# Optimization experiments

Hardware: AMD Instinct MI355X
Metric: run time of the kernel (lower is better)

The kernel has to match this reference:

```python
import jax, jax.numpy as jnp
import numpy as np

B, S, H = 32, 4096, 512

def setup_inputs() -> dict:
    key = jax.random.key(0)
    k1, k2, k3, k4, k5 = jax.random.split(key, 5)
    scale = 1.0 / np.sqrt(H)
    return {
        "query": jax.random.normal(k1, (B, 1, H), dtype=jnp.float32),
        "keys": jax.random.normal(k2, (B, S, H), dtype=jnp.float32),
        "Wa": jax.random.normal(k3, (H, H), dtype=jnp.float32) * scale,
        "Ua": jax.random.normal(k4, (H, H), dtype=jnp.float32) * scale,
        "Va": jax.random.normal(k5, (H, 1), dtype=jnp.float32) * scale,
    }

def reference(query, keys, Wa, Ua, Va):
    # additive (Bahdanau) attention scores: Va^T tanh(Wa q + Ua k)
    q_proj = jnp.einsum('bqh,hd->bqd', query, Wa)          # [B,1,H]
    k_proj = jnp.einsum('bsh,hd->bsd', keys, Ua)           # [B,S,H]
    scores = jnp.einsum('bsd,d->bs', jnp.tanh(q_proj + k_proj), Va[:, 0])  # [B,S]
    weights = jax.nn.softmax(scores, axis=-1)[:, None, :]  # [B,1,S]
    context = jnp.einsum('bqs,bsh->bqh', weights, keys)    # [B,1,H]
    return (context, weights)
```

## Files before the change

### kernel.cpp

```cpp
#include <hip/hip_runtime.h>
#include <hip/hip_bf16.h>

#define B_ 32
#define S_ 4096
#define H_ 512

typedef short bf16x8 __attribute__((ext_vector_type(8)));
typedef unsigned short u16x8 __attribute__((ext_vector_type(8)));
typedef float f32x4 __attribute__((ext_vector_type(4)));

__device__ inline unsigned short f2bf(float x) {
    unsigned u = __float_as_uint(x);
    return (unsigned short)((u + 0x7fffu + ((u >> 16) & 1u)) >> 16);
}

__device__ inline float fast_tanh(float x) {
    float e = __expf(2.f * x);
    return 1.f - 2.f / (e + 1.f);
}

__device__ __forceinline__ void stage16(const void* g, void* lds_base) {
    __builtin_amdgcn_global_load_lds(
        (const __attribute__((address_space(1))) unsigned char*)g,
        (__attribute__((address_space(3))) unsigned char*)lds_base, 16, 0, 0);
}

__global__ void k_prep_ua(const float* __restrict__ Ua,
                          unsigned short* __restrict__ ua_t) {
    __shared__ float tile[32][33];
    int h0 = blockIdx.x * 32, d0 = blockIdx.y * 32;
    int tx = threadIdx.x, ty = threadIdx.y;
#pragma unroll
    for (int j = 0; j < 4; ++j)
        tile[ty + j * 8][tx] = Ua[(size_t)(h0 + ty + j * 8) * H_ + d0 + tx];
    __syncthreads();
#pragma unroll
    for (int j = 0; j < 4; ++j) {
        int dl = ty + j * 8;
        ua_t[(size_t)(d0 + dl) * H_ + h0 + tx] = f2bf(tile[tx][dl]);
    }
}

__global__ __launch_bounds__(512) void k_qproj(const float* __restrict__ query,
                                               const float* __restrict__ Wa,
                                               float* __restrict__ qproj) {
    __shared__ float q[H_];
    int b = blockIdx.x, d = threadIdx.x;
    q[d] = query[(size_t)b * H_ + d];
    __syncthreads();
    float acc = 0.f;
    for (int h = 0; h < H_; ++h)
        acc = fmaf(q[h], Wa[(size_t)h * H_ + d], acc);
    qproj[(size_t)b * H_ + d] = acc;
}

__global__ __launch_bounds__(512, 2) void k_scores(
    const float* __restrict__ keys, const unsigned short* __restrict__ ua_t,
    const float* __restrict__ qproj, const float* __restrict__ Va,
    float* __restrict__ part_sc) {
    __shared__ __align__(16) unsigned char As[2][16384];
    __shared__ __align__(16) unsigned char Bs[2][16384];
    __shared__ float smp[4][128];

    int tid = threadIdx.x;
    int wave = tid >> 6, lane = tid & 63;
    int lq = lane & 15, lh = lane >> 4;
    int wm = wave >> 2;
    int wnn = wave & 3;

    int logical = (blockIdx.x & 7) * 512 + (blockIdx.x >> 3);
    int b  = logical >> 7;
    int m0 = ((logical >> 2) & 31) * 128;
    int nb = logical & 3;

    const float* keysb = keys + (size_t)b * S_ * H_;

    int r = tid >> 2, qtr = tid & 3;
    const float* aptr = keysb + (size_t)(m0 + r) * H_ + qtr * 16;
    unsigned aswz  = (unsigned)((r & 7) << 4);
    unsigned abase = (unsigned)(r * 128);

    int rb0 = wave * 8 + (lane >> 3);
    int rb1 = 64 + rb0;
    unsigned cb = (unsigned)((lane & 7) * 16);
    const unsigned char* uab = (const unsigned char*)ua_t;
    const unsigned char* bsrc0 = uab + ((size_t)(nb * 128 + rb0)) * 1024 + (cb ^ ((rb0 & 7) << 4));
    const unsigned char* bsrc1 = uab + ((size_t)(nb * 128 + rb1)) * 1024 + (cb ^ ((rb1 & 7) << 4));

    f32x4 acc[4][2];
#pragma unroll
    for (int i = 0; i < 4; ++i)
#pragma unroll
        for (int j = 0; j < 2; ++j) acc[i][j] = (f32x4){0.f, 0.f, 0.f, 0.f};

    unsigned swzR = (unsigned)((lq & 7) << 4);

    float4 arg[4];

    stage16(bsrc0, &Bs[0][wave * 1024]);
    stage16(bsrc1, &Bs[0][8192 + wave * 1024]);
#pragma unroll
    for (int j = 0; j < 4; ++j) arg[j] = *(const float4*)(aptr + j * 4);
#pragma unroll
    for (int j16 = 0; j16 < 2; ++j16) {
        float4 x = arg[2 * j16], y = arg[2 * j16 + 1];
        u16x8 v;
        v[0] = f2bf(x.x); v[1] = f2bf(x.y); v[2] = f2bf(x.z); v[3] = f2bf(x.w);
        v[4] = f2bf(y.x); v[5] = f2bf(y.y); v[6] = f2bf(y.z); v[7] = f2bf(y.w);
        *(u16x8*)(&As[0][0] + abase + ((unsigned)(qtr * 32 + j16 * 16) ^ aswz)) = v;
    }
    __syncthreads();

#pragma unroll
    for (int t = 0; t < 8; ++t) {
        const int cur = t & 1, nxt = cur ^ 1;

        if (t < 7) {
            stage16(bsrc0 + (t + 1) * 128, &Bs[nxt][wave * 1024]);
            stage16(bsrc1 + (t + 1) * 128, &Bs[nxt][8192 + wave * 1024]);
#pragma unroll
            for (int j = 0; j < 4; ++j)
                arg[j] = *(const float4*)(aptr + (t + 1) * 64 + j * 4);
        }

#pragma unroll
        for (int ks = 0; ks < 2; ++ks) {
            bf16x8 af[4], bv[2];
            unsigned koff = (unsigned)(ks * 64 + lh * 16) ^ swzR;
#pragma unroll
            for (int mf = 0; mf < 4; ++mf)
                af[mf] = *(const bf16x8*)(&As[cur][0] + (unsigned)((wm * 64 + mf * 16 + lq) * 128) + koff);
#pragma unroll
            for (int nf = 0; nf < 2; ++nf)
                bv[nf] = *(const bf16x8*)(&Bs[cur][0] + (unsigned)((wnn * 32 + nf * 16 + lq) * 128) + koff);
#pragma unroll
            for (int mf = 0; mf < 4; ++mf)
#pragma unroll
                for (int nf = 0; nf < 2; ++nf)
                    acc[mf][nf] = __builtin_amdgcn_mfma_f32_16x16x32_bf16(
                        af[mf], bv[nf], acc[mf][nf], 0, 0, 0);
        }

        if (t < 7) {
#pragma unroll
            for (int j16 = 0; j16 < 2; ++j16) {
                float4 x = arg[2 * j16], y = arg[2 * j16 + 1];
                u16x8 v;
                v[0] = f2bf(x.x); v[1] = f2bf(x.y); v[2] = f2bf(x.z); v[3] = f2bf(x.w);
                v[4] = f2bf(y.x); v[5] = f2bf(y.y); v[6] = f2bf(y.z); v[7] = f2bf(y.w);
                *(u16x8*)(&As[nxt][0] + abase + ((unsigned)(qtr * 32 + j16 * 16) ^ aswz)) = v;
            }
        }

        __syncthreads();
    }

    float va_r[2], qp_r[2];
#pragma unroll
    for (int nf = 0; nf < 2; ++nf) {
        int n = nb * 128 + wnn * 32 + nf * 16 + lq;
        va_r[nf] = Va[n];
        qp_r[nf] = qproj[(size_t)b * H_ + n];
    }
#pragma unroll
    for (int mf = 0; mf < 4; ++mf) {
#pragma unroll
        for (int reg = 0; reg < 4; ++reg) {
            float p = va_r[0] * fast_tanh(qp_r[0] + acc[mf][0][reg])
                    + va_r[1] * fast_tanh(qp_r[1] + acc[mf][1][reg]);
            p += __shfl_xor(p, 1);
            p += __shfl_xor(p, 2);
            p += __shfl_xor(p, 4);
            p += __shfl_xor(p, 8);
            if (lq == 0) smp[wnn][wm * 64 + mf * 16 + lh * 4 + reg] = p;
        }
    }
    __syncthreads();
    if (tid < 128) {
        float s = smp[0][tid] + smp[1][tid] + smp[2][tid] + smp[3][tid];
        part_sc[((size_t)nb * B_ + b) * S_ + m0 + tid] = s;
    }
}

__global__ __launch_bounds__(512) void k_softmax(const float* __restrict__ part_sc,
                                                 float* __restrict__ wts) {
    __shared__ float red[8];
    int b = blockIdx.x, tid = threadIdx.x;
    const float* p0 = part_sc + (size_t)b * S_;
    const float* p1 = p0 + (size_t)B_ * S_;
    const float* p2 = p1 + (size_t)B_ * S_;
    const float* p3 = p2 + (size_t)B_ * S_;
    float v[8];
    float m = -1e30f;
#pragma unroll
    for (int i = 0; i < 8; ++i) {
        int s = tid + i * 512;
        v[i] = ((p0[s] + p1[s]) + (p2[s] + p3[s]));
        m = fmaxf(m, v[i]);
    }
#pragma unroll
    for (int o = 1; o < 64; o <<= 1) m = fmaxf(m, __shfl_xor(m, o));
    if ((tid & 63) == 0) red[tid >> 6] = m;
    __syncthreads();
    m = red[0];
#pragma unroll
    for (int w = 1; w < 8; ++w) m = fmaxf(m, red[w]);
    float sum = 0.f;
#pragma unroll
    for (int i = 0; i < 8; ++i) {
        v[i] = __expf(v[i] - m);
        sum += v[i];
    }
#pragma unroll
    for (int o = 1; o < 64; o <<= 1) sum += __shfl_xor(sum, o);
    __syncthreads();
    if ((tid & 63) == 0) red[tid >> 6] = sum;
    __syncthreads();
    float tot = 0.f;
#pragma unroll
    for (int w = 0; w < 8; ++w) tot += red[w];
    float inv = 1.f / tot;
#pragma unroll
    for (int i = 0; i < 8; ++i) wts[(size_t)b * S_ + tid + i * 512] = v[i] * inv;
}

__global__ __launch_bounds__(512) void k_ctx_part(const float* __restrict__ keys,
                                                  const float* __restrict__ wts,
                                                  float* __restrict__ part) {
    int c = blockIdx.x, b = blockIdx.y, h = threadIdx.x;
    const float* wrow = wts + (size_t)b * S_ + c * 128;
    const float* kbase = keys + ((size_t)b * S_ + c * 128) * H_ + h;
    float acc = 0.f;
#pragma unroll 8
    for (int s = 0; s < 128; ++s)
        acc = fmaf(wrow[s], kbase[(size_t)s * H_], acc);
    part[((size_t)c * B_ + b) * H_ + h] = acc;
}

__global__ __launch_bounds__(512) void k_ctx_reduce(const float* __restrict__ part,
                                                    float* __restrict__ ctx) {
    int b = blockIdx.x, h = threadIdx.x;
    float s = 0.f;
#pragma unroll
    for (int c = 0; c < 32; ++c) s += part[((size_t)c * B_ + b) * H_ + h];
    ctx[(size_t)b * H_ + h] = s;
}

extern "C" void kernel_launch(void* const* d_in, const int* in_sizes, int n_in,
                              void* d_out, int out_size, void* d_ws, size_t ws_size,
                              hipStream_t stream) {
    const float* query = (const float*)d_in[0];
    const float* keys  = (const float*)d_in[1];
    const float* Wa    = (const float*)d_in[2];
    const float* Ua    = (const float*)d_in[3];
    const float* Va    = (const float*)d_in[4];

    float* out = (float*)d_out;
    float* ctx = out;
    float* wts = out + B_ * H_;

    char* ws = (char*)d_ws;
    unsigned short* ua_t = (unsigned short*)ws;
    float* qproj   = (float*)(ws + 524288);
    float* part_sc = (float*)(ws + 524288 + 65536);
    float* part_cx = (float*)(ws + 524288 + 65536 + 2097152);

    k_prep_ua<<<dim3(16, 16), dim3(32, 8), 0, stream>>>(Ua, ua_t);
    k_qproj<<<dim3(32), dim3(512), 0, stream>>>(query, Wa, qproj);
    k_scores<<<dim3(4096), dim3(512), 0, stream>>>(keys, ua_t, qproj, Va, part_sc);
    k_softmax<<<dim3(32), dim3(512), 0, stream>>>(part_sc, wts);
    k_ctx_part<<<dim3(32, 32), dim3(512), 0, stream>>>(keys, wts, part_cx);
    k_ctx_reduce<<<dim3(32), dim3(512), 0, stream>>>(part_cx, ctx);
}
```

Measured before the change: 215.9 us.

## Halve scores block to 256 threads with 4x4 MFMA tiles per wave

The scores GEMM block drops from 8 to 4 waves. Each wave now computes a 64x64 tile (4x4 MFMA fragments) instead of 64x32, which raises register-level reuse of the A and B fragments per LDS read. The keys tile in LDS is single-buffered to save shared memory, which allows 3 blocks per CU. The cost is an extra barrier per k-step and fewer threads to hide global load latency, and each thread now loads twice as much A data per step.

```diff
diff --git a/kernel.cpp b/kernel.cpp
--- a/kernel.cpp
+++ b/kernel.cpp
@@ -54,19 +54,18 @@
     qproj[(size_t)b * H_ + d] = acc;
 }
 
-__global__ __launch_bounds__(512, 2) void k_scores(
+__global__ __launch_bounds__(256, 3) void k_scores(
     const float* __restrict__ keys, const unsigned short* __restrict__ ua_t,
     const float* __restrict__ qproj, const float* __restrict__ Va,
     float* __restrict__ part_sc) {
-    __shared__ __align__(16) unsigned char As[2][16384];
+    __shared__ __align__(16) unsigned char As[16384];
     __shared__ __align__(16) unsigned char Bs[2][16384];
-    __shared__ float smp[4][128];
+    __shared__ float smp[2][128];
 
     int tid = threadIdx.x;
     int wave = tid >> 6, lane = tid & 63;
     int lq = lane & 15, lh = lane >> 4;
-    int wm = wave >> 2;
-    int wnn = wave & 3;
+    int wm = wave >> 1, wn = wave & 1;
 
     int logical = (blockIdx.x & 7) * 512 + (blockIdx.x >> 3);
     int b  = logical >> 7;
@@ -75,90 +74,97 @@
 
     const float* keysb = keys + (size_t)b * S_ * H_;
 
-    int r = tid >> 2, qtr = tid & 3;
-    const float* aptr = keysb + (size_t)(m0 + r) * H_ + qtr * 16;
-    unsigned aswz  = (unsigned)((r & 7) << 4);
-    unsigned abase = (unsigned)(r * 128);
-
-    int rb0 = wave * 8 + (lane >> 3);
-    int rb1 = 64 + rb0;
-    unsigned cb = (unsigned)((lane & 7) * 16);
+    int r = tid >> 1, hh = tid & 1;
+    const float* aptr = keysb + (size_t)(m0 + r) * H_ + hh * 32;
+    unsigned aswz = (unsigned)((r & 7) << 4);
+    unsigned arow = (unsigned)(r * 128);
+
+    int rbl = lane >> 3;
+    unsigned cb = (unsigned)(((lane & 7) * 16) ^ (rbl << 4));
     const unsigned char* uab = (const unsigned char*)ua_t;
-    const unsigned char* bsrc0 = uab + ((size_t)(nb * 128 + rb0)) * 1024 + (cb ^ ((rb0 & 7) << 4));
-    const unsigned char* bsrc1 = uab + ((size_t)(nb * 128 + rb1)) * 1024 + (cb ^ ((rb1 & 7) << 4));
-
-    f32x4 acc[4][2];
+    const unsigned char* bsrc[4];
+    unsigned bdst[4];
+#pragma unroll
+    for (int i = 0; i < 4; ++i) {
+        int j = wave * 4 + i;
+        bsrc[i] = uab + ((size_t)(nb * 128 + 8 * j + rbl)) * 1024 + cb;
+        bdst[i] = (unsigned)(j * 1024);
+    }
+
+    f32x4 acc[4][4];
 #pragma unroll
     for (int i = 0; i < 4; ++i)
 #pragma unroll
-        for (int j = 0; j < 2; ++j) acc[i][j] = (f32x4){0.f, 0.f, 0.f, 0.f};
-
-    unsigned swzR = (unsigned)((lq & 7) << 4);
-
-    float4 arg[4];
-
-    stage16(bsrc0, &Bs[0][wave * 1024]);
-    stage16(bsrc1, &Bs[0][8192 + wave * 1024]);
-#pragma unroll
-    for (int j = 0; j < 4; ++j) arg[j] = *(const float4*)(aptr + j * 4);
-#pragma unroll
-    for (int j16 = 0; j16 < 2; ++j16) {
-        float4 x = arg[2 * j16], y = arg[2 * j16 + 1];
-        u16x8 v;
-        v[0] = f2bf(x.x); v[1] = f2bf(x.y); v[2] = f2bf(x.z); v[3] = f2bf(x.w);
-        v[4] = f2bf(y.x); v[5] = f2bf(y.y); v[6] = f2bf(y.z); v[7] = f2bf(y.w);
-        *(u16x8*)(&As[0][0] + abase + ((unsigned)(qtr * 32 + j16 * 16) ^ aswz)) = v;
+        for (int j = 0; j < 4; ++j) acc[i][j] = (f32x4){0.f, 0.f, 0.f, 0.f};
+
+#pragma unroll
+    for (int i = 0; i < 4; ++i) stage16(bsrc[i], &Bs[0][bdst[i]]);
+    {
+        float4 a0[8];
+#pragma unroll
+        for (int j = 0; j < 8; ++j) a0[j] = *(const float4*)(aptr + j * 4);
+#pragma unroll
+        for (int j16 = 0; j16 < 4; ++j16) {
+            float4 x = a0[2 * j16], y = a0[2 * j16 + 1];
+            u16x8 v;
+            v[0] = f2bf(x.x); v[1] = f2bf(x.y); v[2] = f2bf(x.z); v[3] = f2bf(x.w);
+            v[4] = f2bf(y.x); v[5] = f2bf(y.y); v[6] = f2bf(y.z); v[7] = f2bf(y.w);
+            *(u16x8*)(As + arow + ((unsigned)(hh * 64 + j16 * 16) ^ aswz)) = v;
+        }
     }
     __syncthreads();
 
 #pragma unroll
     for (int t = 0; t < 8; ++t) {
         const int cur = t & 1, nxt = cur ^ 1;
-
+        float4 ar[8];
         if (t < 7) {
-            stage16(bsrc0 + (t + 1) * 128, &Bs[nxt][wave * 1024]);
-            stage16(bsrc1 + (t + 1) * 128, &Bs[nxt][8192 + wave * 1024]);
-#pragma unroll
-            for (int j = 0; j < 4; ++j)
-                arg[j] = *(const float4*)(aptr + (t + 1) * 64 + j * 4);
-        }
-
+#pragma unroll
+            for (int i = 0; i < 4; ++i)
+                stage16(bsrc[i] + (t + 1) * 128, &Bs[nxt][bdst[i]]);
+#pragma unroll
+            for (int j = 0; j < 8; ++j)
+                ar[j] = *(const float4*)(aptr + (t + 1) * 64 + j * 4);
+        }
 #pragma unroll
         for (int ks = 0; ks < 2; ++ks) {
-            bf16x8 af[4], bv[2];
-            unsigned koff = (unsigned)(ks * 64 + lh * 16) ^ swzR;
+            bf16x8 af[4], bv[4];
+            unsigned koff = (unsigned)(ks * 64 + lh * 16);
+#pragma unroll
+            for (int mf = 0; mf < 4; ++mf) {
+                unsigned R = (unsigned)(wm * 64 + mf * 16 + lq);
+                af[mf] = *(const bf16x8*)(As + R * 128 + (koff ^ ((R & 7) << 4)));
+            }
+#pragma unroll
+            for (int nf = 0; nf < 4; ++nf) {
+                unsigned R = (unsigned)(wn * 64 + nf * 16 + lq);
+                bv[nf] = *(const bf16x8*)(&Bs[cur][0] + R * 128 + (koff ^ ((R & 7) << 4)));
+            }
 #pragma unroll
             for (int mf = 0; mf < 4; ++mf)
-                af[mf] = *(const bf16x8*)(&As[cur][0] + (unsigned)((wm * 64 + mf * 16 + lq) * 128) + koff);
-#pragma unroll
-            for (int nf = 0; nf < 2; ++nf)
-                bv[nf] = *(const bf16x8*)(&Bs[cur][0] + (unsigned)((wnn * 32 + nf * 16 + lq) * 128) + koff);
-#pragma unroll
-            for (int mf = 0; mf < 4; ++mf)
-#pragma unroll
-                for (int nf = 0; nf < 2; ++nf)
+#pragma unroll
+                for (int nf = 0; nf < 4; ++nf)
                     acc[mf][nf] = __builtin_amdgcn_mfma_f32_16x16x32_bf16(
                         af[mf], bv[nf], acc[mf][nf], 0, 0, 0);
         }
-
+        __syncthreads();
         if (t < 7) {
 #pragma unroll
-            for (int j16 = 0; j16 < 2; ++j16) {
-                float4 x = arg[2 * j16], y = arg[2 * j16 + 1];
+            for (int j16 = 0; j16 < 4; ++j16) {
+                float4 x = ar[2 * j16], y = ar[2 * j16 + 1];
                 u16x8 v;
                 v[0] = f2bf(x.x); v[1] = f2bf(x.y); v[2] = f2bf(x.z); v[3] = f2bf(x.w);
                 v[4] = f2bf(y.x); v[5] = f2bf(y.y); v[6] = f2bf(y.z); v[7] = f2bf(y.w);
-                *(u16x8*)(&As[nxt][0] + abase + ((unsigned)(qtr * 32 + j16 * 16) ^ aswz)) = v;
+                *(u16x8*)(As + arow + ((unsigned)(hh * 64 + j16 * 16) ^ aswz)) = v;
             }
-        }
-
-        __syncthreads();
-    }
-
-    float va_r[2], qp_r[2];
-#pragma unroll
-    for (int nf = 0; nf < 2; ++nf) {
-        int n = nb * 128 + wnn * 32 + nf * 16 + lq;
+            __syncthreads();
+        }
+    }
+
+    float va_r[4], qp_r[4];
+#pragma unroll
+    for (int nf = 0; nf < 4; ++nf) {
+        int n = nb * 128 + wn * 64 + nf * 16 + lq;
         va_r[nf] = Va[n];
         qp_r[nf] = qproj[(size_t)b * H_ + n];
     }
@@ -166,18 +172,20 @@
     for (int mf = 0; mf < 4; ++mf) {
 #pragma unroll
         for (int reg = 0; reg < 4; ++reg) {
-            float p = va_r[0] * fast_tanh(qp_r[0] + acc[mf][0][reg])
-                    + va_r[1] * fast_tanh(qp_r[1] + acc[mf][1][reg]);
+            float p = 0.f;
+#pragma unroll
+            for (int nf = 0; nf < 4; ++nf)
+                p += va_r[nf] * fast_tanh(qp_r[nf] + acc[mf][nf][reg]);
             p += __shfl_xor(p, 1);
             p += __shfl_xor(p, 2);
             p += __shfl_xor(p, 4);
             p += __shfl_xor(p, 8);
-            if (lq == 0) smp[wnn][wm * 64 + mf * 16 + lh * 4 + reg] = p;
+            if (lq == 0) smp[wn][wm * 64 + mf * 16 + lh * 4 + reg] = p;
         }
     }
     __syncthreads();
     if (tid < 128) {
-        float s = smp[0][tid] + smp[1][tid] + smp[2][tid] + smp[3][tid];
+        float s = smp[0][tid] + smp[1][tid];
         part_sc[((size_t)nb * B_ + b) * S_ + m0 + tid] = s;
     }
 }
@@ -267,7 +275,7 @@
 
     k_prep_ua<<<dim3(16, 16), dim3(32, 8), 0, stream>>>(Ua, ua_t);
     k_qproj<<<dim3(32), dim3(512), 0, stream>>>(query, Wa, qproj);
-    k_scores<<<dim3(4096), dim3(512), 0, stream>>>(keys, ua_t, qproj, Va, part_sc);
+    k_scores<<<dim3(4096), dim3(256), 0, stream>>>(keys, ua_t, qproj, Va, part_sc);
     k_softmax<<<dim3(32), dim3(512), 0, stream>>>(part_sc, wts);
     k_ctx_part<<<dim3(32, 32), dim3(512), 0, stream>>>(keys, wts, part_cx);
     k_ctx_reduce<<<dim3(32), dim3(512), 0, stream>>>(part_cx, ctx);
```

Result: slower. 246.1 us (+14.0%).

## Make k_scores persistent over eight M-tiles with continuous pipelined K loop

Applied to the files above, without the earlier changes.

k_scores now launches 512 blocks instead of 4096. Each block walks eight 128-row M-tiles of a 1024-row chunk in a single double-buffered loop of 64 steps, so the pipeline keeps running across tile boundaries. The epilogue that applies tanh, multiplies by Va and writes partial scores now runs every eight steps inside the loop. Float-to-bf16 conversion uses the packed bf16x2 intrinsic, the A staging layout changes, and launch bounds are raised to 4 blocks per CU. The intent is to cut per-block prologue and tail costs and to keep loads overlapping across tiles. The risks are that 512 blocks may underfill the GPU, and that the in-loop epilogue adds a sync and register pressure.

```diff
diff --git a/kernel.cpp b/kernel.cpp
--- a/kernel.cpp
+++ b/kernel.cpp
@@ -6,12 +6,16 @@
 #define H_ 512
 
 typedef short bf16x8 __attribute__((ext_vector_type(8)));
-typedef unsigned short u16x8 __attribute__((ext_vector_type(8)));
 typedef float f32x4 __attribute__((ext_vector_type(4)));
 
 __device__ inline unsigned short f2bf(float x) {
     unsigned u = __float_as_uint(x);
     return (unsigned short)((u + 0x7fffu + ((u >> 16) & 1u)) >> 16);
+}
+
+__device__ __forceinline__ unsigned cvt2(float a, float b) {
+    __hip_bfloat162 h = __float22bfloat162_rn(float2{a, b});
+    return *reinterpret_cast<unsigned*>(&h);
 }
 
 __device__ inline float fast_tanh(float x) {
@@ -54,7 +58,7 @@
     qproj[(size_t)b * H_ + d] = acc;
 }
 
-__global__ __launch_bounds__(512, 2) void k_scores(
+__global__ __launch_bounds__(512, 4) void k_scores(
     const float* __restrict__ keys, const unsigned short* __restrict__ ua_t,
     const float* __restrict__ qproj, const float* __restrict__ Va,
     float* __restrict__ part_sc) {
@@ -68,91 +72,27 @@
     int wm = wave >> 2;
     int wnn = wave & 3;
 
-    int logical = (blockIdx.x & 7) * 512 + (blockIdx.x >> 3);
-    int b  = logical >> 7;
-    int m0 = ((logical >> 2) & 31) * 128;
+    int logical = (blockIdx.x & 7) * 64 + (blockIdx.x >> 3);
     int nb = logical & 3;
-
-    const float* keysb = keys + (size_t)b * S_ * H_;
-
-    int r = tid >> 2, qtr = tid & 3;
-    const float* aptr = keysb + (size_t)(m0 + r) * H_ + qtr * 16;
-    unsigned aswz  = (unsigned)((r & 7) << 4);
-    unsigned abase = (unsigned)(r * 128);
-
-    int rb0 = wave * 8 + (lane >> 3);
-    int rb1 = 64 + rb0;
-    unsigned cb = (unsigned)((lane & 7) * 16);
+    int bm = logical >> 2;
+    int b = bm >> 2;
+    int mchunk = bm & 3;
+    const float* keysb = keys + ((size_t)b * S_ + (size_t)mchunk * 1024) * H_;
+
+    int ar = tid >> 4;
+    int acf = (tid & 15) * 4;
+    unsigned awb = (unsigned)(((tid & 15) * 8) ^ ((ar & 7) << 4));
+
+    int rbl = lane >> 3;
+    unsigned cbb = (unsigned)(((lane & 7) * 16) ^ (rbl << 4));
     const unsigned char* uab = (const unsigned char*)ua_t;
-    const unsigned char* bsrc0 = uab + ((size_t)(nb * 128 + rb0)) * 1024 + (cb ^ ((rb0 & 7) << 4));
-    const unsigned char* bsrc1 = uab + ((size_t)(nb * 128 + rb1)) * 1024 + (cb ^ ((rb1 & 7) << 4));
-
-    f32x4 acc[4][2];
-#pragma unroll
-    for (int i = 0; i < 4; ++i)
-#pragma unroll
-        for (int j = 0; j < 2; ++j) acc[i][j] = (f32x4){0.f, 0.f, 0.f, 0.f};
-
-    unsigned swzR = (unsigned)((lq & 7) << 4);
-
-    float4 arg[4];
-
-    stage16(bsrc0, &Bs[0][wave * 1024]);
-    stage16(bsrc1, &Bs[0][8192 + wave * 1024]);
-#pragma unroll
-    for (int j = 0; j < 4; ++j) arg[j] = *(const float4*)(aptr + j * 4);
-#pragma unroll
-    for (int j16 = 0; j16 < 2; ++j16) {
-        float4 x = arg[2 * j16], y = arg[2 * j16 + 1];
-        u16x8 v;
-        v[0] = f2bf(x.x); v[1] = f2bf(x.y); v[2] = f2bf(x.z); v[3] = f2bf(x.w);
-        v[4] = f2bf(y.x); v[5] = f2bf(y.y); v[6] = f2bf(y.z); v[7] = f2bf(y.w);
-        *(u16x8*)(&As[0][0] + abase + ((unsigned)(qtr * 32 + j16 * 16) ^ aswz)) = v;
-    }
-    __syncthreads();
-
-#pragma unroll
-    for (int t = 0; t < 8; ++t) {
-        const int cur = t & 1, nxt = cur ^ 1;
-
-        if (t < 7) {
-            stage16(bsrc0 + (t + 1) * 128, &Bs[nxt][wave * 1024]);
-            stage16(bsrc1 + (t + 1) * 128, &Bs[nxt][8192 + wave * 1024]);
-#pragma unroll
-            for (int j = 0; j < 4; ++j)
-                arg[j] = *(const float4*)(aptr + (t + 1) * 64 + j * 4);
-        }
-
-#pragma unroll
-        for (int ks = 0; ks < 2; ++ks) {
-            bf16x8 af[4], bv[2];
-            unsigned koff = (unsigned)(ks * 64 + lh * 16) ^ swzR;
-#pragma unroll
-            for (int mf = 0; mf < 4; ++mf)
-                af[mf] = *(const bf16x8*)(&As[cur][0] + (unsigned)((wm * 64 + mf * 16 + lq) * 128) + koff);
-#pragma unroll
-            for (int nf = 0; nf < 2; ++nf)
-                bv[nf] = *(const bf16x8*)(&Bs[cur][0] + (unsigned)((wnn * 32 + nf * 16 + lq) * 128) + koff);
-#pragma unroll
-            for (int mf = 0; mf < 4; ++mf)
-#pragma unroll
-                for (int nf = 0; nf < 2; ++nf)
-                    acc[mf][nf] = __builtin_amdgcn_mfma_f32_16x16x32_bf16(
-                        af[mf], bv[nf], acc[mf][nf], 0, 0, 0);
-        }
-
-        if (t < 7) {
-#pragma unroll
-            for (int j16 = 0; j16 < 2; ++j16) {
-                float4 x = arg[2 * j16], y = arg[2 * j16 + 1];
-                u16x8 v;
-                v[0] = f2bf(x.x); v[1] = f2bf(x.y); v[2] = f2bf(x.z); v[3] = f2bf(x.w);
-                v[4] = f2bf(y.x); v[5] = f2bf(y.y); v[6] = f2bf(y.z); v[7] = f2bf(y.w);
-                *(u16x8*)(&As[nxt][0] + abase + ((unsigned)(qtr * 32 + j16 * 16) ^ aswz)) = v;
-            }
-        }
-
-        __syncthreads();
+    const unsigned char* bsrc[2];
+    unsigned bdst[2];
+#pragma unroll
+    for (int i = 0; i < 2; ++i) {
+        int j = wave * 2 + i;
+        bsrc[i] = uab + ((size_t)(nb * 128 + 8 * j + rbl)) * 1024 + cbb;
+        bdst[i] = (unsigned)(j * 1024);
     }
 
     float va_r[2], qp_r[2];
@@ -162,23 +102,98 @@
         va_r[nf] = Va[n];
         qp_r[nf] = qproj[(size_t)b * H_ + n];
     }
-#pragma unroll
-    for (int mf = 0; mf < 4; ++mf) {
-#pragma unroll
-        for (int reg = 0; reg < 4; ++reg) {
-            float p = va_r[0] * fast_tanh(qp_r[0] + acc[mf][0][reg])
-                    + va_r[1] * fast_tanh(qp_r[1] + acc[mf][1][reg]);
-            p += __shfl_xor(p, 1);
-            p += __shfl_xor(p, 2);
-            p += __shfl_xor(p, 4);
-            p += __shfl_xor(p, 8);
-            if (lq == 0) smp[wnn][wm * 64 + mf * 16 + lh * 4 + reg] = p;
-        }
-    }
-    __syncthreads();
-    if (tid < 128) {
-        float s = smp[0][tid] + smp[1][tid] + smp[2][tid] + smp[3][tid];
-        part_sc[((size_t)nb * B_ + b) * S_ + m0 + tid] = s;
+
+    f32x4 acc[4][2];
+#pragma unroll
+    for (int i = 0; i < 4; ++i)
+#pragma unroll
+        for (int j = 0; j < 2; ++j) acc[i][j] = (f32x4){0.f, 0.f, 0.f, 0.f};
+
+#pragma unroll
+    for (int i = 0; i < 2; ++i) stage16(bsrc[i], &Bs[0][bdst[i]]);
+    {
+        const float* ap = keysb + (size_t)ar * H_ + acf;
+#pragma unroll
+        for (int s = 0; s < 4; ++s) {
+            float4 v = *(const float4*)(ap + (size_t)(32 * s) * H_);
+            uint2 w;
+            w.x = cvt2(v.x, v.y);
+            w.y = cvt2(v.z, v.w);
+            *(uint2*)(&As[0][0] + (unsigned)((ar + 32 * s) * 128) + awb) = w;
+        }
+    }
+    __syncthreads();
+
+#pragma unroll 2
+    for (int g = 0; g < 64; ++g) {
+        const int cur = g & 1, nxt = cur ^ 1;
+        float4 av[4];
+        if (g < 63) {
+            int g1 = g + 1;
+            int kk1 = g1 & 7, mt1 = g1 >> 3;
+#pragma unroll
+            for (int i = 0; i < 2; ++i)
+                stage16(bsrc[i] + kk1 * 128, &Bs[nxt][bdst[i]]);
+            const float* ap = keysb + (size_t)(mt1 * 128 + ar) * H_ + kk1 * 64 + acf;
+#pragma unroll
+            for (int s = 0; s < 4; ++s)
+                av[s] = *(const float4*)(ap + (size_t)(32 * s) * H_);
+        }
+#pragma unroll
+        for (int ks = 0; ks < 2; ++ks) {
+            bf16x8 af[4], bv[2];
+            unsigned koff = (unsigned)(ks * 64 + lh * 16);
+#pragma unroll
+            for (int mf = 0; mf < 4; ++mf) {
+                unsigned R = (unsigned)(wm * 64 + mf * 16 + lq);
+                af[mf] = *(const bf16x8*)(&As[cur][0] + R * 128 + (koff ^ ((R & 7) << 4)));
+            }
+#pragma unroll
+            for (int nf = 0; nf < 2; ++nf) {
+                unsigned R = (unsigned)(wnn * 32 + nf * 16 + lq);
+                bv[nf] = *(const bf16x8*)(&Bs[cur][0] + R * 128 + (koff ^ ((R & 7) << 4)));
+            }
+#pragma unroll
+            for (int mf = 0; mf < 4; ++mf)
+#pragma unroll
+                for (int nf = 0; nf < 2; ++nf)
+                    acc[mf][nf] = __builtin_amdgcn_mfma_f32_16x16x32_bf16(
+                        af[mf], bv[nf], acc[mf][nf], 0, 0, 0);
+        }
+        if (g < 63) {
+#pragma unroll
+            for (int s = 0; s < 4; ++s) {
+                uint2 w;
+                w.x = cvt2(av[s].x, av[s].y);
+                w.y = cvt2(av[s].z, av[s].w);
+                *(uint2*)(&As[nxt][0] + (unsigned)((ar + 32 * s) * 128) + awb) = w;
+            }
+        }
+        __syncthreads();
+        if ((g & 7) == 7) {
+            int mt = g >> 3;
+#pragma unroll
+            for (int mf = 0; mf < 4; ++mf) {
+#pragma unroll
+                for (int reg = 0; reg < 4; ++reg) {
+                    float p = va_r[0] * fast_tanh(qp_r[0] + acc[mf][0][reg])
+                            + va_r[1] * fast_tanh(qp_r[1] + acc[mf][1][reg]);
+                    p += __shfl_xor(p, 1);
+                    p += __shfl_xor(p, 2);
+                    p += __shfl_xor(p, 4);
+                    p += __shfl_xor(p, 8);
+                    if (lq == 0) smp[wnn][wm * 64 + mf * 16 + lh * 4 + reg] = p;
+                }
+#pragma unroll
+                for (int nf = 0; nf < 2; ++nf)
+                    acc[mf][nf] = (f32x4){0.f, 0.f, 0.f, 0.f};
+            }
+            __syncthreads();
+            if (tid < 128) {
+                float s = smp[0][tid] + smp[1][tid] + smp[2][tid] + smp[3][tid];
+                part_sc[((size_t)nb * B_ + b) * S_ + mchunk * 1024 + mt * 128 + tid] = s;
+            }
+        }
     }
 }
 
@@ -267,7 +282,7 @@
 
     k_prep_ua<<<dim3(16, 16), dim3(32, 8), 0, stream>>>(Ua, ua_t);
     k_qproj<<<dim3(32), dim3(512), 0, stream>>>(query, Wa, qproj);
-    k_scores<<<dim3(4096), dim3(512), 0, stream>>>(keys, ua_t, qproj, Va, part_sc);
+    k_scores<<<dim3(512), dim3(512), 0, stream>>>(keys, ua_t, qproj, Va, part_sc);
     k_softmax<<<dim3(32), dim3(512), 0, stream>>>(part_sc, wts);
     k_ctx_part<<<dim3(32, 32), dim3(512), 0, stream>>>(keys, wts, part_cx);
     k_ctx_reduce<<<dim3(32), dim3(512), 0, stream>>>(part_cx, ctx);
```

Result: faster. 211.4 us (-2.1%).
